# Optimization experiments

Measured on AMD Instinct MI355X. Metric: run time of the kernel, lower is better.

## Reference

```python
import jax, jax.numpy as jnp
import numpy as np

C = 1024   # hidden_size
H = 16     # num_heads
D = C // H # head dim
M = 4096   # mlp hidden
T = 1024   # motion seq len
B = 8      # batch
TA = 1024  # audio seq len


def _w(key, shape):
    return jax.random.normal(key, shape, dtype=jnp.float32) * 0.02


def setup_inputs() -> dict:
    key = jax.random.key(0)
    ks = jax.random.split(key, 32)
    inp = {
        'x': jax.random.normal(ks[0], (T, B, C), dtype=jnp.float32),
        'c': jax.random.normal(ks[1], (B, C), dtype=jnp.float32),
        'padding_mask': jax.random.randint(ks[2], (B, T), 0, 2, dtype=jnp.int32),
        'audio_seq': jax.random.normal(ks[3], (TA, B, C), dtype=jnp.float32),
        'audio_mask': jax.random.randint(ks[4], (B, TA), 0, 2, dtype=jnp.int32),
        # adaLN modulation: SiLU -> Linear(C, 6C)
        'w_ada': _w(ks[5], (C, 6 * C)), 'b_ada': jnp.zeros((6 * C,), jnp.float32),
        # self-attention q/k/v/proj
        'wq': _w(ks[6], (C, C)), 'bq': jnp.zeros((C,), jnp.float32),
        'wk': _w(ks[7], (C, C)), 'bk': jnp.zeros((C,), jnp.float32),
        'wv': _w(ks[8], (C, C)), 'bv': jnp.zeros((C,), jnp.float32),
        'wo': _w(ks[9], (C, C)), 'bo': jnp.zeros((C,), jnp.float32),
        # cross-attention q/k/v/proj
        'cwq': _w(ks[10], (C, C)), 'cbq': jnp.zeros((C,), jnp.float32),
        'cwk': _w(ks[11], (C, C)), 'cbk': jnp.zeros((C,), jnp.float32),
        'cwv': _w(ks[12], (C, C)), 'cbv': jnp.zeros((C,), jnp.float32),
        'cwo': _w(ks[13], (C, C)), 'cbo': jnp.zeros((C,), jnp.float32),
        # MLP fc1/fc2
        'w1': _w(ks[14], (C, M)), 'b1': jnp.zeros((M,), jnp.float32),
        'w2': _w(ks[15], (M, C)), 'b2': jnp.zeros((C,), jnp.float32),
    }
    return inp


def _ln(x):
    # LayerNorm(elementwise_affine=False, eps=1e-6)
    mu = jnp.mean(x, axis=-1, keepdims=True)
    var = jnp.var(x, axis=-1, keepdims=True)
    return (x - mu) * jax.lax.rsqrt(var + 1e-6)


def _modulate(x, shift, scale):
    # batch-first x [B, T, C]; shift/scale [B, C]
    return x * (1.0 + scale[:, None, :]) + shift[:, None, :]


def _mha(xq, xkv, wq, bq, wk, bk, wv, bv, wo, bo, mask):
    # xq [B, Tq, C], xkv [B, Tk, C], mask [B, Tk] (nonzero = masked)
    b, tq, _ = xq.shape
    tk = xkv.shape[1]
    q = (xq @ wq + bq).reshape(b, tq, H, D)
    k = (xkv @ wk + bk).reshape(b, tk, H, D)
    v = (xkv @ wv + bv).reshape(b, tk, H, D)
    att = jnp.einsum('bqhd,bkhd->bhqk', q, k) * (1.0 / np.sqrt(D))
    att = jnp.where(mask[:, None, None, :] != 0, -jnp.inf, att)
    att = jax.nn.softmax(att, axis=-1)
    y = jnp.einsum('bhqk,bkhd->bqhd', att, v).reshape(b, tq, C)
    return y @ wo + bo


def _gelu_tanh(x):
    return jax.nn.gelu(x, approximate=True)


def reference(x, c, padding_mask, audio_seq, audio_mask,
              w_ada, b_ada, wq, bq, wk, bk, wv, bv, wo, bo,
              cwq, cbq, cwk, cbk, cwv, cbv, cwo, cbo,
              w1, b1, w2, b2):
    # adaLN modulation parameters
    mod = jax.nn.silu(c) @ w_ada + b_ada                 # [B, 6C]
    (shift_msa, scale_msa, gate_msa,
     shift_mlp, scale_mlp, gate_mlp) = jnp.split(mod, 6, axis=1)

    # x is sequence-first [T, B, C] (padding_mask batch dim matches x dim 1)
    x_batch = jnp.transpose(x, (1, 0, 2))                # [B, T, C]
    x_mod = _modulate(_ln(x_batch), shift_msa, scale_msa)
    attn_out = _mha(x_mod, x_mod, wq, bq, wk, bk, wv, bv, wo, bo, padding_mask)
    x = x + gate_msa[None, :, :] * jnp.transpose(attn_out, (1, 0, 2))

    # cross attention (reuses msa shift/scale/gate, as in the source)
    xb = jnp.transpose(x, (1, 0, 2))                     # [B, T, C]
    ab = jnp.transpose(audio_seq, (1, 0, 2))             # [B, TA, C]
    x_cross_in = _modulate(_ln(xb), shift_msa, scale_msa)
    cross_out = _mha(x_cross_in, ab, cwq, cbq, cwk, cbk, cwv, cbv, cwo, cbo,
                     audio_mask)
    x = x + gate_msa[None, :, :] * jnp.transpose(cross_out, (1, 0, 2))

    # MLP
    xb = jnp.transpose(x, (1, 0, 2))
    h = _modulate(_ln(xb), shift_mlp, scale_mlp)
    mlp_out = _gelu_tanh(h @ w1 + b1) @ w2 + b2
    x = x + gate_mlp[None, :, :] * jnp.transpose(mlp_out, (1, 0, 2))
    return x
```

## Files before the change

kernel.cpp:

```cpp
#include <hip/hip_runtime.h>
#include <math.h>

#define T_SEQ 1024
#define TA_SEQ 1024
#define BATCH 8
#define CH 1024
#define NH 16
#define HD 64
#define MH 4096

typedef unsigned short u16;
typedef unsigned short u16x4 __attribute__((ext_vector_type(4)));
typedef unsigned short u16x8 __attribute__((ext_vector_type(8)));
typedef __bf16 bf16x8 __attribute__((ext_vector_type(8)));
typedef float f32x4 __attribute__((ext_vector_type(4)));

__device__ __forceinline__ u16 f2bf(float f) {
  unsigned int u = __builtin_bit_cast(unsigned int, f);
  u += 0x7FFFu + ((u >> 16) & 1u);
  return (u16)(u >> 16);
}
__device__ __forceinline__ u16 f2bf_trunc(float f) {
  return (u16)(__builtin_bit_cast(unsigned int, f) >> 16);
}
__device__ __forceinline__ bf16x8 ldbf8(const u16* p) {
  return __builtin_bit_cast(bf16x8, *reinterpret_cast<const u16x8*>(p));
}
__device__ __forceinline__ void gload_lds16(const u16* g, u16* l) {
  __builtin_amdgcn_global_load_lds(
      (const __attribute__((address_space(1))) unsigned int*)g,
      (__attribute__((address_space(3))) unsigned int*)l, 16, 0, 0);
}

__global__ void k_transpose_w(const float* __restrict__ in, u16* __restrict__ out,
                              int K, int N) {
  __shared__ float tile[32][33];
  int n0 = blockIdx.x * 32, k0 = blockIdx.y * 32;
  int tx = threadIdx.x, ty = threadIdx.y;
#pragma unroll
  for (int i = 0; i < 4; i++)
    tile[ty + i * 8][tx] = in[(size_t)(k0 + ty + i * 8) * N + n0 + tx];
  __syncthreads();
#pragma unroll
  for (int i = 0; i < 4; i++)
    out[(size_t)(n0 + ty + i * 8) * K + k0 + tx] = f2bf(tile[tx][ty + i * 8]);
}

struct P8f { const float* p[8]; };
struct P8u { u16* p[8]; };
__global__ void k_transpose8(P8f in8, P8u out8) {
  const float* __restrict__ in = in8.p[blockIdx.z];
  u16* __restrict__ out = out8.p[blockIdx.z];
  __shared__ float tile[32][33];
  int n0 = blockIdx.x * 32, k0 = blockIdx.y * 32;
  int tx = threadIdx.x, ty = threadIdx.y;
#pragma unroll
  for (int i = 0; i < 4; i++)
    tile[ty + i * 8][tx] = in[(size_t)(k0 + ty + i * 8) * CH + n0 + tx];
  __syncthreads();
#pragma unroll
  for (int i = 0; i < 4; i++)
    out[(size_t)(n0 + ty + i * 8) * CH + k0 + tx] = f2bf(tile[tx][ty + i * 8]);
}

__global__ void k_ada(const float* __restrict__ c, const float* __restrict__ w_ada,
                      const float* __restrict__ b_ada, float* __restrict__ mod) {
  __shared__ float sc[CH];
  int b = blockIdx.y;
  int tid = threadIdx.x;
  for (int i = tid; i < CH; i += 256) {
    float cv = c[b * CH + i];
    sc[i] = cv / (1.0f + expf(-cv));
  }
  __syncthreads();
  int n = blockIdx.x * 256 + tid;
  float acc = 0.0f;
  for (int k = 0; k < CH; k++) acc += sc[k] * w_ada[(size_t)k * (6 * CH) + n];
  mod[(size_t)b * (6 * CH) + n] = acc + b_ada[n];
}

__global__ void k_tbc_to_btc_f32(const float* __restrict__ in, float* __restrict__ out) {
  size_t i = (size_t)blockIdx.x * 256 + threadIdx.x;
  int c = (int)(i & (CH - 1));
  size_t tb = i >> 10;
  int b = (int)(tb & (BATCH - 1));
  size_t t = tb >> 3;
  out[((size_t)b * T_SEQ + t) * CH + c] = in[i];
}
__global__ void k_tbc_to_btc_bf16(const float* __restrict__ in, u16* __restrict__ out) {
  size_t i = (size_t)blockIdx.x * 256 + threadIdx.x;
  int c = (int)(i & (CH - 1));
  size_t tb = i >> 10;
  int b = (int)(tb & (BATCH - 1));
  size_t t = tb >> 3;
  out[((size_t)b * TA_SEQ + t) * CH + c] = f2bf(in[i]);
}

__global__ void k_ln_mod(const float* __restrict__ xb, const float* __restrict__ mod,
                         u16* __restrict__ out, int shift_sel, int scale_sel) {
  int row = blockIdx.x;
  int b = row >> 10;
  int tid = threadIdx.x;
  const float* xr = xb + (size_t)row * CH;
  float4 v = reinterpret_cast<const float4*>(xr)[tid];
  float s = v.x + v.y + v.z + v.w;
  float s2 = v.x * v.x + v.y * v.y + v.z * v.z + v.w * v.w;
#pragma unroll
  for (int off = 32; off > 0; off >>= 1) {
    s += __shfl_down(s, off);
    s2 += __shfl_down(s2, off);
  }
  __shared__ float red[8];
  __shared__ float stats[2];
  int wid = tid >> 6;
  if ((tid & 63) == 0) { red[wid] = s; red[4 + wid] = s2; }
  __syncthreads();
  if (tid == 0) {
    float a = red[0] + red[1] + red[2] + red[3];
    float a2 = red[4] + red[5] + red[6] + red[7];
    float mu = a * (1.0f / CH);
    float var = a2 * (1.0f / CH) - mu * mu;
    stats[0] = mu;
    stats[1] = rsqrtf(var + 1e-6f);
  }
  __syncthreads();
  float mu = stats[0], rs = stats[1];
  int c0 = tid * 4;
  const float* sh = mod + (size_t)b * (6 * CH) + (size_t)shift_sel * CH + c0;
  const float* scl = mod + (size_t)b * (6 * CH) + (size_t)scale_sel * CH + c0;
  float xs[4] = {v.x, v.y, v.z, v.w};
  u16x4 o;
#pragma unroll
  for (int j = 0; j < 4; j++)
    o[j] = f2bf((xs[j] - mu) * rs * (1.0f + scl[j]) + sh[j]);
  *reinterpret_cast<u16x4*>(out + (size_t)row * CH + c0) = o;
}

__device__ __forceinline__ void gemm_core(
    const u16* __restrict__ A, const u16* __restrict__ Bt, int K,
    int m0, int n0, int tid, u16* As, u16* Bs, f32x4 (&acc)[4][4]) {
  int wid = tid >> 6, lane = tid & 63;
  int wm = (wid >> 1) * 64, wn = (wid & 1) * 64;
  int lrow = lane & 15, quad = lane >> 4;
  int c0 = tid, c1 = 256 + tid;
  const u16* ga0 = A + (size_t)(m0 + (c0 >> 2)) * K + (c0 & 3) * 8;
  const u16* ga1 = A + (size_t)(m0 + (c1 >> 2)) * K + (c1 & 3) * 8;
  const u16* gb0 = Bt + (size_t)(n0 + (c0 >> 2)) * K + (c0 & 3) * 8;
  const u16* gb1 = Bt + (size_t)(n0 + (c1 >> 2)) * K + (c1 & 3) * 8;
  u16* la0 = As + c0 * 8;
  u16* la1 = As + c1 * 8;
  u16* lb0 = Bs + c0 * 8;
  u16* lb1 = Bs + c1 * 8;
  const int kiters = K >> 5;
  for (int kt = 0; kt < kiters; kt++) {
    int k0 = kt << 5;
    __syncthreads();
    gload_lds16(ga0 + k0, la0);
    gload_lds16(ga1 + k0, la1);
    gload_lds16(gb0 + k0, lb0);
    gload_lds16(gb1 + k0, lb1);
    __syncthreads();
    bf16x8 af[4], bfr[4];
#pragma unroll
    for (int mi = 0; mi < 4; mi++)
      af[mi] = ldbf8(&As[(wm + mi * 16 + lrow) * 32 + quad * 8]);
#pragma unroll
    for (int ni = 0; ni < 4; ni++)
      bfr[ni] = ldbf8(&Bs[(wn + ni * 16 + lrow) * 32 + quad * 8]);
#pragma unroll
    for (int mi = 0; mi < 4; mi++)
#pragma unroll
      for (int ni = 0; ni < 4; ni++)
        acc[mi][ni] = __builtin_amdgcn_mfma_f32_16x16x32_bf16(af[mi], bfr[ni],
                                                              acc[mi][ni], 0, 0, 0);
  }
}

template <int EPI>
__global__ __launch_bounds__(256) void k_gemm(
    const u16* __restrict__ A, const u16* __restrict__ Bt,
    const float* __restrict__ bias, u16* __restrict__ out_bf,
    float* __restrict__ xb, const float* __restrict__ mod, int gate_sel,
    int M, int N, int K) {
  __shared__ u16 As[128 * 32];
  __shared__ u16 Bs[128 * 32];
  int m0 = blockIdx.x * 128, n0 = blockIdx.y * 128;
  int tid = threadIdx.x;
  int wid = tid >> 6, lane = tid & 63;
  int wm = (wid >> 1) * 64, wn = (wid & 1) * 64;
  int lrow = lane & 15, quad = lane >> 4;
  f32x4 acc[4][4];
#pragma unroll
  for (int mi = 0; mi < 4; mi++)
#pragma unroll
    for (int ni = 0; ni < 4; ni++) acc[mi][ni] = {0.f, 0.f, 0.f, 0.f};
  gemm_core(A, Bt, K, m0, n0, tid, As, Bs, acc);
#pragma unroll
  for (int mi = 0; mi < 4; mi++)
#pragma unroll
    for (int ni = 0; ni < 4; ni++) {
      int col = n0 + wn + ni * 16 + lrow;
      float bval = bias[col];
#pragma unroll
      for (int r = 0; r < 4; r++) {
        int row = m0 + wm + mi * 16 + quad * 4 + r;
        float v = acc[mi][ni][r] + bval;
        if (EPI == 1) {
          int b = row >> 10;
          float g = mod[(size_t)b * (6 * CH) + (size_t)gate_sel * CH + col];
          xb[(size_t)row * N + col] += g * v;
        } else if (EPI == 2) {
          float t = 0.79788456080286536f * (v + 0.044715f * v * v * v);
          float gel = 0.5f * v * (1.0f + tanhf(t));
          out_bf[(size_t)row * N + col] = f2bf(gel);
        } else {
          out_bf[(size_t)row * N + col] = f2bf(v * 0.18033688011112042f);
        }
      }
    }
}

__global__ __launch_bounds__(256) void k_gemm_qkv(
    const u16* __restrict__ A, const u16* __restrict__ Bt,
    const float* __restrict__ bq, const float* __restrict__ bk,
    const float* __restrict__ bv,
    u16* __restrict__ qout, u16* __restrict__ kout, u16* __restrict__ vt) {
  __shared__ u16 As[128 * 32];
  __shared__ u16 Bs[128 * 32];
  int m0 = blockIdx.x * 128, n0 = blockIdx.y * 128;
  int tid = threadIdx.x;
  int wid = tid >> 6, lane = tid & 63;
  int wm = (wid >> 1) * 64, wn = (wid & 1) * 64;
  int lrow = lane & 15, quad = lane >> 4;
  f32x4 acc[4][4];
#pragma unroll
  for (int mi = 0; mi < 4; mi++)
#pragma unroll
    for (int ni = 0; ni < 4; ni++) acc[mi][ni] = {0.f, 0.f, 0.f, 0.f};
  gemm_core(A, Bt, CH, m0, n0, tid, As, Bs, acc);
  int seg = n0 >> 10;
  const float* bias = (seg == 0) ? bq : (seg == 1) ? bk : bv;
#pragma unroll
  for (int mi = 0; mi < 4; mi++)
#pragma unroll
    for (int ni = 0; ni < 4; ni++) {
      int col = (n0 & 1023) + wn + ni * 16 + lrow;
      float bval = bias[col];
      int row0 = m0 + wm + mi * 16 + quad * 4;
      if (seg == 0) {
#pragma unroll
        for (int r = 0; r < 4; r++)
          qout[(size_t)(row0 + r) * CH + col] =
              f2bf((acc[mi][ni][r] + bval) * 0.18033688011112042f);
      } else if (seg == 1) {
#pragma unroll
        for (int r = 0; r < 4; r++)
          kout[(size_t)(row0 + r) * CH + col] = f2bf(acc[mi][ni][r] + bval);
      } else {
        u16x4 pk;
#pragma unroll
        for (int r = 0; r < 4; r++) pk[r] = f2bf(acc[mi][ni][r] + bval);
        int b = row0 >> 10, t0 = row0 & 1023;
        int h = col >> 6, d = col & 63;
        *reinterpret_cast<u16x4*>(
            vt + (((size_t)(b * NH + h) * HD + d) << 10) + t0) = pk;
      }
    }
}

__global__ __launch_bounds__(256) void k_gemm_kv(
    const u16* __restrict__ A, const u16* __restrict__ Bt,
    const float* __restrict__ bk, const float* __restrict__ bv,
    u16* __restrict__ kout, u16* __restrict__ vt) {
  __shared__ u16 As[128 * 32];
  __shared__ u16 Bs[128 * 32];
  int m0 = blockIdx.x * 128, n0 = blockIdx.y * 128;
  int tid = threadIdx.x;
  int wid = tid >> 6, lane = tid & 63;
  int wm = (wid >> 1) * 64, wn = (wid & 1) * 64;
  int lrow = lane & 15, quad = lane >> 4;
  f32x4 acc[4][4];
#pragma unroll
  for (int mi = 0; mi < 4; mi++)
#pragma unroll
    for (int ni = 0; ni < 4; ni++) acc[mi][ni] = {0.f, 0.f, 0.f, 0.f};
  gemm_core(A, Bt, CH, m0, n0, tid, As, Bs, acc);
  int seg = n0 >> 10;
  const float* bias = (seg == 0) ? bk : bv;
#pragma unroll
  for (int mi = 0; mi < 4; mi++)
#pragma unroll
    for (int ni = 0; ni < 4; ni++) {
      int col = (n0 & 1023) + wn + ni * 16 + lrow;
      float bval = bias[col];
      int row0 = m0 + wm + mi * 16 + quad * 4;
      if (seg == 0) {
#pragma unroll
        for (int r = 0; r < 4; r++)
          kout[(size_t)(row0 + r) * CH + col] = f2bf(acc[mi][ni][r] + bval);
      } else {
        u16x4 pk;
#pragma unroll
        for (int r = 0; r < 4; r++) pk[r] = f2bf(acc[mi][ni][r] + bval);
        int b = row0 >> 10, t0 = row0 & 1023;
        int h = col >> 6, d = col & 63;
        *reinterpret_cast<u16x4*>(
            vt + (((size_t)(b * NH + h) * HD + d) << 10) + t0) = pk;
      }
    }
}

__global__ __launch_bounds__(256, 2) void k_attn(
    const u16* __restrict__ Q, const u16* __restrict__ Kb,
    const u16* __restrict__ vt, const int* __restrict__ mask,
    u16* __restrict__ Y) {
  int qt = blockIdx.x, h = blockIdx.y, b = blockIdx.z;
  int tid = threadIdx.x, wid = tid >> 6, lane = tid & 63;
  int lrow = lane & 15, quad = lane >> 4;
  int qbase = qt * 256 + wid * 64;

  __shared__ u16 P[4][4][16][72];

  bf16x8 aq[4][2];
#pragma unroll
  for (int st = 0; st < 4; st++) {
    size_t qoff = ((size_t)(b * T_SEQ + qbase + st * 16 + lrow)) * CH + h * HD;
    aq[st][0] = ldbf8(Q + qoff + quad * 8);
    aq[st][1] = ldbf8(Q + qoff + 32 + quad * 8);
  }

  u16x8 uo;
#pragma unroll
  for (int j = 0; j < 8; j++) uo[j] = (lrow == 0) ? (u16)0x3F80 : (u16)0;
  bf16x8 ones = __builtin_bit_cast(bf16x8, uo);

  const int* mrow = mask + (size_t)b * T_SEQ;
  const u16* ksrc = Kb + ((size_t)(b * T_SEQ) + lrow) * CH + h * HD + quad * 8;
  const u16* vsrc = vt + (((size_t)(b * NH + h) * HD + lrow) << 10) + quad * 8;

  f32x4 o[4][5];
#pragma unroll
  for (int st = 0; st < 4; st++)
#pragma unroll
    for (int dc = 0; dc < 5; dc++) o[st][dc] = {0.f, 0.f, 0.f, 0.f};

  for (int kt = 0; kt < 16; kt++) {
    int kb = kt * 64;
    bf16x8 kf[8];
    float mb[4];
#pragma unroll
    for (int sub = 0; sub < 4; sub++) {
      const u16* kp = ksrc + (size_t)(kb + sub * 16) * CH;
      kf[sub * 2] = ldbf8(kp);
      kf[sub * 2 + 1] = ldbf8(kp + 32);
      mb[sub] = mrow[kb + sub * 16 + lrow] ? -INFINITY : 0.0f;
    }
    bf16x8 vf[8];
#pragma unroll
    for (int dc = 0; dc < 4; dc++) {
      const u16* vp = vsrc + (size_t)(dc * 16) * 1024 + kb;
      vf[dc * 2] = ldbf8(vp);
      vf[dc * 2 + 1] = ldbf8(vp + 32);
    }
#pragma unroll
    for (int st = 0; st < 4; st++) {
#pragma unroll
      for (int sub = 0; sub < 4; sub++) {
        f32x4 z = {0.f, 0.f, 0.f, 0.f};
        z = __builtin_amdgcn_mfma_f32_16x16x32_bf16(aq[st][0], kf[sub * 2], z, 0, 0, 0);
        z = __builtin_amdgcn_mfma_f32_16x16x32_bf16(aq[st][1], kf[sub * 2 + 1], z, 0, 0, 0);
        float mbv = mb[sub];
#pragma unroll
        for (int r = 0; r < 4; r++) {
          float p = exp2f(z[r] + mbv);
          P[wid][st][quad * 4 + r][sub * 16 + lrow] = f2bf_trunc(p);
        }
      }
    }
#pragma unroll
    for (int st = 0; st < 4; st++) {
      bf16x8 pf0 = ldbf8(&P[wid][st][lrow][quad * 8]);
      bf16x8 pf1 = ldbf8(&P[wid][st][lrow][32 + quad * 8]);
#pragma unroll
      for (int dc = 0; dc < 4; dc++) {
        o[st][dc] = __builtin_amdgcn_mfma_f32_16x16x32_bf16(pf0, vf[dc * 2], o[st][dc], 0, 0, 0);
        o[st][dc] = __builtin_amdgcn_mfma_f32_16x16x32_bf16(pf1, vf[dc * 2 + 1], o[st][dc], 0, 0, 0);
      }
      o[st][4] = __builtin_amdgcn_mfma_f32_16x16x32_bf16(pf0, ones, o[st][4], 0, 0, 0);
      o[st][4] = __builtin_amdgcn_mfma_f32_16x16x32_bf16(pf1, ones, o[st][4], 0, 0, 0);
    }
  }

#pragma unroll
  for (int st = 0; st < 4; st++)
#pragma unroll
    for (int r = 0; r < 4; r++) {
      float l = __shfl(o[st][4][r], lane & 48);
      float linv = 1.0f / l;
      int qr = qbase + st * 16 + quad * 4 + r;
      size_t yo = ((size_t)(b * T_SEQ + qr)) * CH + h * HD;
#pragma unroll
      for (int dc = 0; dc < 4; dc++)
        Y[yo + dc * 16 + lrow] = f2bf(o[st][dc][r] * linv);
    }
}

__global__ void k_out(const float* __restrict__ xb, float* __restrict__ out) {
  size_t i = (size_t)blockIdx.x * 256 + threadIdx.x;
  int c = (int)(i & (CH - 1));
  size_t tb = i >> 10;
  int b = (int)(tb & (BATCH - 1));
  size_t t = tb >> 3;
  out[i] = xb[((size_t)b * T_SEQ + t) * CH + c];
}

extern "C" void kernel_launch(void* const* d_in, const int* in_sizes, int n_in,
                              void* d_out, int out_size, void* d_ws, size_t ws_size,
                              hipStream_t stream) {
  const float* x     = (const float*)d_in[0];
  const float* c     = (const float*)d_in[1];
  const int*   pmask = (const int*)d_in[2];
  const float* audio = (const float*)d_in[3];
  const int*   amask = (const int*)d_in[4];
  const float* w_ada = (const float*)d_in[5];
  const float* b_ada = (const float*)d_in[6];
  const float* wq = (const float*)d_in[7];  const float* bq = (const float*)d_in[8];
  const float* wk = (const float*)d_in[9];  const float* bk = (const float*)d_in[10];
  const float* wv = (const float*)d_in[11]; const float* bv = (const float*)d_in[12];
  const float* wo = (const float*)d_in[13]; const float* bo = (const float*)d_in[14];
  const float* cwq = (const float*)d_in[15]; const float* cbq = (const float*)d_in[16];
  const float* cwk = (const float*)d_in[17]; const float* cbk = (const float*)d_in[18];
  const float* cwv = (const float*)d_in[19]; const float* cbv = (const float*)d_in[20];
  const float* cwo = (const float*)d_in[21]; const float* cbo = (const float*)d_in[22];
  const float* w1 = (const float*)d_in[23]; const float* b1 = (const float*)d_in[24];
  const float* w2 = (const float*)d_in[25]; const float* b2 = (const float*)d_in[26];

  char* wsb = (char*)d_ws;
  size_t off = 0;
  auto alloc = [&](size_t bytes) {
    char* p = wsb + off;
    off += (bytes + 255) & ~(size_t)255;
    return p;
  };
  const size_t SQ = (size_t)CH * CH * 2;
  u16* wqT  = (u16*)alloc(SQ);
  u16* wkT  = (u16*)alloc(SQ);
  u16* wvT  = (u16*)alloc(SQ);
  u16* woT  = (u16*)alloc(SQ);
  u16* cwqT = (u16*)alloc(SQ);
  u16* cwkT = (u16*)alloc(SQ);
  u16* cwvT = (u16*)alloc(SQ);
  u16* cwoT = (u16*)alloc(SQ);
  u16* w1T  = (u16*)alloc((size_t)CH * MH * 2);
  u16* w2T  = (u16*)alloc((size_t)CH * MH * 2);
  float* mod = (float*)alloc((size_t)BATCH * 6 * CH * 4);
  float* xb  = (float*)alloc((size_t)BATCH * T_SEQ * CH * 4);
  u16* xm    = (u16*)alloc((size_t)BATCH * T_SEQ * CH * 2);
  u16* hbuf  = (u16*)alloc((size_t)BATCH * T_SEQ * MH * 2);
  u16* qbuf  = hbuf;
  u16* kbuf  = hbuf + (size_t)BATCH * T_SEQ * CH;
  u16* ybuf  = hbuf + (size_t)2 * BATCH * T_SEQ * CH;
  u16* vt    = hbuf + (size_t)3 * BATCH * T_SEQ * CH;
  u16* abuf  = (u16*)alloc((size_t)BATCH * TA_SEQ * CH * 2);
  (void)ws_size; (void)in_sizes; (void)n_in; (void)out_size;

  const int NE = T_SEQ * BATCH * CH;
  dim3 tb32(32, 8);

  P8f src8; P8u dst8;
  src8.p[0] = wq;  dst8.p[0] = wqT;
  src8.p[1] = wk;  dst8.p[1] = wkT;
  src8.p[2] = wv;  dst8.p[2] = wvT;
  src8.p[3] = wo;  dst8.p[3] = woT;
  src8.p[4] = cwq; dst8.p[4] = cwqT;
  src8.p[5] = cwk; dst8.p[5] = cwkT;
  src8.p[6] = cwv; dst8.p[6] = cwvT;
  src8.p[7] = cwo; dst8.p[7] = cwoT;
  k_transpose8<<<dim3(CH / 32, CH / 32, 8), tb32, 0, stream>>>(src8, dst8);
  k_transpose_w<<<dim3(MH / 32, CH / 32), tb32, 0, stream>>>(w1, w1T, CH, MH);
  k_transpose_w<<<dim3(CH / 32, MH / 32), tb32, 0, stream>>>(w2, w2T, MH, CH);

  k_ada<<<dim3(6 * CH / 256, BATCH), 256, 0, stream>>>(c, w_ada, b_ada, mod);
  k_tbc_to_btc_f32<<<NE / 256, 256, 0, stream>>>(x, xb);
  k_tbc_to_btc_bf16<<<NE / 256, 256, 0, stream>>>(audio, abuf);

  k_ln_mod<<<BATCH * T_SEQ, 256, 0, stream>>>(xb, mod, xm, 0, 1);
  k_gemm_qkv<<<dim3(64, 24), 256, 0, stream>>>(xm, wqT, bq, bk, bv, qbuf, kbuf, vt);
  k_attn<<<dim3(T_SEQ / 256, NH, BATCH), 256, 0, stream>>>(qbuf, kbuf, vt, pmask, ybuf);
  k_gemm<1><<<dim3(64, 8), 256, 0, stream>>>(ybuf, woT, bo, nullptr, xb, mod, 2, 8192, CH, CH);

  k_ln_mod<<<BATCH * T_SEQ, 256, 0, stream>>>(xb, mod, xm, 0, 1);
  k_gemm<3><<<dim3(64, 8), 256, 0, stream>>>(xm, cwqT, cbq, qbuf, nullptr, nullptr, 0, 8192, CH, CH);
  k_gemm_kv<<<dim3(64, 16), 256, 0, stream>>>(abuf, cwkT, cbk, cbv, kbuf, vt);
  k_attn<<<dim3(T_SEQ / 256, NH, BATCH), 256, 0, stream>>>(qbuf, kbuf, vt, amask, ybuf);
  k_gemm<1><<<dim3(64, 8), 256, 0, stream>>>(ybuf, cwoT, cbo, nullptr, xb, mod, 2, 8192, CH, CH);

  k_ln_mod<<<BATCH * T_SEQ, 256, 0, stream>>>(xb, mod, xm, 3, 4);
  k_gemm<2><<<dim3(64, 32), 256, 0, stream>>>(xm, w1T, b1, hbuf, nullptr, nullptr, 0, 8192, MH, CH);
  k_gemm<1><<<dim3(64, 8), 256, 0, stream>>>(hbuf, w2T, b2, nullptr, xb, mod, 5, 8192, CH, MH);

  k_out<<<NE / 256, 256, 0, stream>>>(xb, (float*)d_out);
}
```

Baseline: 968.5 us.

## Double-buffer GEMM LDS tiles and XOR-swizzle shared memory layout

The shared GEMM core now uses two LDS buffers per operand. The global-to-LDS loads for the next K slice are issued before the MFMA work on the current slice, so memory latency overlaps with compute and the loop needs fewer barriers. The LDS layout is also XOR-swizzled across the four 8-element chunks of each row, applied on the global-load side and undone on the fragment reads, to cut LDS bank conflicts. In exchange, LDS use per block doubles, which may lower occupancy, and the loop now assumes an even number of K iterations.

```diff
diff --git a/kernel.cpp b/kernel.cpp
--- a/kernel.cpp
+++ b/kernel.cpp
@@ -136,43 +136,68 @@
   *reinterpret_cast<u16x4*>(out + (size_t)row * CH + c0) = o;
 }
 
+__device__ __forceinline__ void gemm_compute(const u16* As, const u16* Bs,
+                                             int wm, int wn, int lrow, int sx,
+                                             f32x4 (&acc)[4][4]) {
+  bf16x8 af[4], bfr[4];
+#pragma unroll
+  for (int mi = 0; mi < 4; mi++)
+    af[mi] = ldbf8(&As[(wm + mi * 16 + lrow) * 32 + sx]);
+#pragma unroll
+  for (int ni = 0; ni < 4; ni++)
+    bfr[ni] = ldbf8(&Bs[(wn + ni * 16 + lrow) * 32 + sx]);
+#pragma unroll
+  for (int mi = 0; mi < 4; mi++)
+#pragma unroll
+    for (int ni = 0; ni < 4; ni++)
+      acc[mi][ni] = __builtin_amdgcn_mfma_f32_16x16x32_bf16(af[mi], bfr[ni],
+                                                            acc[mi][ni], 0, 0, 0);
+}
+
 __device__ __forceinline__ void gemm_core(
     const u16* __restrict__ A, const u16* __restrict__ Bt, int K,
     int m0, int n0, int tid, u16* As, u16* Bs, f32x4 (&acc)[4][4]) {
   int wid = tid >> 6, lane = tid & 63;
   int wm = (wid >> 1) * 64, wn = (wid & 1) * 64;
   int lrow = lane & 15, quad = lane >> 4;
+  int sx = (quad ^ ((lrow >> 1) & 3)) * 8;
   int c0 = tid, c1 = 256 + tid;
-  const u16* ga0 = A + (size_t)(m0 + (c0 >> 2)) * K + (c0 & 3) * 8;
-  const u16* ga1 = A + (size_t)(m0 + (c1 >> 2)) * K + (c1 & 3) * 8;
-  const u16* gb0 = Bt + (size_t)(n0 + (c0 >> 2)) * K + (c0 & 3) * 8;
-  const u16* gb1 = Bt + (size_t)(n0 + (c1 >> 2)) * K + (c1 & 3) * 8;
+  int r0 = c0 >> 2, r1 = c1 >> 2;
+  int q0 = ((c0 & 3) ^ ((r0 >> 1) & 3)) * 8;
+  int q1 = ((c1 & 3) ^ ((r1 >> 1) & 3)) * 8;
+  const u16* ga0 = A + (size_t)(m0 + r0) * K + q0;
+  const u16* ga1 = A + (size_t)(m0 + r1) * K + q1;
+  const u16* gb0 = Bt + (size_t)(n0 + r0) * K + q0;
+  const u16* gb1 = Bt + (size_t)(n0 + r1) * K + q1;
   u16* la0 = As + c0 * 8;
   u16* la1 = As + c1 * 8;
   u16* lb0 = Bs + c0 * 8;
   u16* lb1 = Bs + c1 * 8;
   const int kiters = K >> 5;
-  for (int kt = 0; kt < kiters; kt++) {
-    int k0 = kt << 5;
+  gload_lds16(ga0, la0);
+  gload_lds16(ga1, la1);
+  gload_lds16(gb0, lb0);
+  gload_lds16(gb1, lb1);
+  __syncthreads();
+  for (int kt = 0; kt < kiters; kt += 2) {
+    {
+      int ke = (kt + 1) << 5;
+      gload_lds16(ga0 + ke, la0 + 4096);
+      gload_lds16(ga1 + ke, la1 + 4096);
+      gload_lds16(gb0 + ke, lb0 + 4096);
+      gload_lds16(gb1 + ke, lb1 + 4096);
+    }
+    gemm_compute(As, Bs, wm, wn, lrow, sx, acc);
     __syncthreads();
-    gload_lds16(ga0 + k0, la0);
-    gload_lds16(ga1 + k0, la1);
-    gload_lds16(gb0 + k0, lb0);
-    gload_lds16(gb1 + k0, lb1);
-    __syncthreads();
-    bf16x8 af[4], bfr[4];
-#pragma unroll
-    for (int mi = 0; mi < 4; mi++)
-      af[mi] = ldbf8(&As[(wm + mi * 16 + lrow) * 32 + quad * 8]);
-#pragma unroll
-    for (int ni = 0; ni < 4; ni++)
-      bfr[ni] = ldbf8(&Bs[(wn + ni * 16 + lrow) * 32 + quad * 8]);
-#pragma unroll
-    for (int mi = 0; mi < 4; mi++)
-#pragma unroll
-      for (int ni = 0; ni < 4; ni++)
-        acc[mi][ni] = __builtin_amdgcn_mfma_f32_16x16x32_bf16(af[mi], bfr[ni],
-                                                              acc[mi][ni], 0, 0, 0);
+    if (kt + 2 < kiters) {
+      int ko = (kt + 2) << 5;
+      gload_lds16(ga0 + ko, la0);
+      gload_lds16(ga1 + ko, la1);
+      gload_lds16(gb0 + ko, lb0);
+      gload_lds16(gb1 + ko, lb1);
+    }
+    gemm_compute(As + 4096, Bs + 4096, wm, wn, lrow, sx, acc);
+    if (kt + 2 < kiters) __syncthreads();
   }
 }
 
@@ -182,8 +207,8 @@
     const float* __restrict__ bias, u16* __restrict__ out_bf,
     float* __restrict__ xb, const float* __restrict__ mod, int gate_sel,
     int M, int N, int K) {
-  __shared__ u16 As[128 * 32];
-  __shared__ u16 Bs[128 * 32];
+  __shared__ u16 As[2 * 128 * 32];
+  __shared__ u16 Bs[2 * 128 * 32];
   int m0 = blockIdx.x * 128, n0 = blockIdx.y * 128;
   int tid = threadIdx.x;
   int wid = tid >> 6, lane = tid & 63;
@@ -225,8 +250,8 @@
     const float* __restrict__ bq, const float* __restrict__ bk,
     const float* __restrict__ bv,
     u16* __restrict__ qout, u16* __restrict__ kout, u16* __restrict__ vt) {
-  __shared__ u16 As[128 * 32];
-  __shared__ u16 Bs[128 * 32];
+  __shared__ u16 As[2 * 128 * 32];
+  __shared__ u16 Bs[2 * 128 * 32];
   int m0 = blockIdx.x * 128, n0 = blockIdx.y * 128;
   int tid = threadIdx.x;
   int wid = tid >> 6, lane = tid & 63;
@@ -272,8 +297,8 @@
     const u16* __restrict__ A, const u16* __restrict__ Bt,
     const float* __restrict__ bk, const float* __restrict__ bv,
     u16* __restrict__ kout, u16* __restrict__ vt) {
-  __shared__ u16 As[128 * 32];
-  __shared__ u16 Bs[128 * 32];
+  __shared__ u16 As[2 * 128 * 32];
+  __shared__ u16 Bs[2 * 128 * 32];
   int m0 = blockIdx.x * 128, n0 = blockIdx.y * 128;
   int tid = threadIdx.x;
   int wid = tid >> 6, lane = tid & 63;
```

New measurement: 1.010 ms. 1.04x slower.
